# Optimization experiments

Measured on AMD Instinct MI355X. Metric: run time of the kernel, lower is better.

Reference implementation:

```python
import jax, jax.numpy as jnp
import numpy as np

PAD = 26
H = 1900
B = 256
T_EPI = 25
T_ANT = 64
T_TOT = 153
EMB = 10
IC = 2 * H  # classifier in_channels = 3800


def setup_inputs() -> dict:
    key = jax.random.key(0)
    ks = jax.random.split(key, 16)
    def rn(i, s, sc):
        return jax.random.normal(ks[i], s, jnp.float32) * sc
    inp = {
        "epitope_x": jax.random.randint(ks[0], (B, T_EPI), 0, 26),
        "left_antigen_x": jax.random.randint(ks[1], (B, T_ANT), 0, 26),
        "right_antigen_x": jax.random.randint(ks[2], (B, T_ANT), 0, 26),
        "total_antigen_x": jax.random.randint(ks[3], (B, T_TOT), 0, 26),
        "embed": rn(4, (27, EMB), 0.1),
        "wx": rn(5, (EMB, 4 * H), 0.1),
        "wh": rn(6, (H, 4 * H), 0.02),
        "wmx": rn(7, (EMB, H), 0.1),
        "wmh": rn(8, (H, H), 0.02),
        "b": rn(9, (4 * H,), 0.1),
        "gx": jnp.ones((4 * H,), jnp.float32),
        "gh": jnp.ones((4 * H,), jnp.float32),
        "gmx": jnp.ones((H,), jnp.float32),
        "gmh": jnp.ones((H,), jnp.float32),
        "bn1_gamma": jnp.ones((IC,), jnp.float32),
        "bn1_beta": jnp.zeros((IC,), jnp.float32),
        "bn1_mean": jnp.zeros((IC,), jnp.float32),
        "bn1_var": jnp.ones((IC,), jnp.float32),
        "W1": rn(10, (IC, IC // 10), 0.02),
        "b1": jnp.zeros((IC // 10,), jnp.float32),
        "bn2_gamma": jnp.ones((IC // 10,), jnp.float32),
        "bn2_beta": jnp.zeros((IC // 10,), jnp.float32),
        "bn2_mean": jnp.zeros((IC // 10,), jnp.float32),
        "bn2_var": jnp.ones((IC // 10,), jnp.float32),
        "W2": rn(11, (IC // 10, 1), 0.05),
        "b2": jnp.zeros((1,), jnp.float32),
    }
    return inp


def _wn(w, g):
    # tf.nn.l2_normalize(w, dim=0) * g  (eps 1e-12)
    return w * (g * jax.lax.rsqrt(jnp.maximum(jnp.sum(w * w, axis=0, keepdims=True), 1e-12)))


def _mlstm(xs, wx, wh, wmx, wmh, b):
    # xs: [T, B, E] -> hidden states [B, T, H]
    nB = xs.shape[1]
    def step(carry, x):
        c, h = carry
        m = (x @ wmx) * (h @ wmh)
        z = x @ wx + m @ wh + b
        i, f, o, u = jnp.split(z, 4, axis=1)
        c = jax.nn.sigmoid(f) * c + jax.nn.sigmoid(i) * jnp.tanh(u)
        h = jax.nn.sigmoid(o) * jnp.tanh(c)
        return (c, h), h
    init = (jnp.zeros((nB, H), xs.dtype), jnp.zeros((nB, H), xs.dtype))
    _, hs = jax.lax.scan(step, init, xs)
    return jnp.swapaxes(hs, 0, 1)


def _forward(epitope_x, left_antigen_x, right_antigen_x, total_antigen_x, embed,
             wx, wh, wmx, wmh, b, gx, gh, gmx, gmh,
             bn1_gamma, bn1_beta, bn1_mean, bn1_var, W1, b1,
             bn2_gamma, bn2_beta, bn2_mean, bn2_var, W2, b2):
    wxn = _wn(wx, gx); whn = _wn(wh, gh); wmxn = _wn(wmx, gmx); wmhn = _wn(wmh, gmh)
    epi_len = jnp.sum((epitope_x != PAD).astype(jnp.int32), axis=1)
    left_len = jnp.maximum(jnp.sum((left_antigen_x != PAD).astype(jnp.int32), axis=1), 1)
    right_len = jnp.maximum(jnp.sum((right_antigen_x != PAD).astype(jnp.int32), axis=1), 1)
    tot_len = epi_len + left_len + right_len
    epi_emb = embed[epitope_x]          # [B, 25, 10]
    tot_emb = embed[total_antigen_x]    # [B, 153, 10]
    epi_hs = _mlstm(jnp.swapaxes(epi_emb, 0, 1), wxn, whn, wmxn, wmhn, b)   # [B, 25, H]
    tot_hs = _mlstm(jnp.swapaxes(tot_emb, 0, 1), wxn, whn, wmxn, wmhn, b)   # [B, 153, H]
    ei = jnp.clip(epi_len - 1, 0, epi_hs.shape[1] - 1)
    ti = jnp.clip(tot_len - 1, 0, tot_hs.shape[1] - 1)
    epi_h = jnp.take_along_axis(epi_hs, ei[:, None, None], axis=1)[:, 0]
    tot_h = jnp.take_along_axis(tot_hs, ti[:, None, None], axis=1)[:, 0]
    x = jnp.concatenate([tot_h, epi_h], axis=-1)  # [B, 3800]
    lrelu = lambda v: jnp.where(v >= 0, v, 0.3 * v)
    bn = lambda v, g, bt, m, vv: (v - m) * jax.lax.rsqrt(vv + 1e-3) * g + bt
    x = bn(lrelu(x), bn1_gamma, bn1_beta, bn1_mean, bn1_var)
    x = x @ W1 + b1
    x = bn(lrelu(x), bn2_gamma, bn2_beta, bn2_mean, bn2_var)
    x = x @ W2 + b2
    return x.reshape(-1)


def reference(epitope_x, left_antigen_x, right_antigen_x, total_antigen_x, embed,
              wx, wh, wmx, wmh, b, gx, gh, gmx, gmh,
              bn1_gamma, bn1_beta, bn1_mean, bn1_var, W1, b1,
              bn2_gamma, bn2_beta, bn2_mean, bn2_var, W2, b2):
    return _forward(epitope_x, left_antigen_x, right_antigen_x, total_antigen_x, embed,
                    wx, wh, wmx, wmh, b, gx, gh, gmx, gmh,
                    bn1_gamma, bn1_beta, bn1_mean, bn1_var, W1, b1,
                    bn2_gamma, bn2_beta, bn2_mean, bn2_var, W2, b2)
```

## Files before the change

kernel.cpp:

```cpp
#include <hip/hip_runtime.h>


typedef _Float16 f16;
typedef _Float16 half8 __attribute__((ext_vector_type(8)));
typedef float f32x4 __attribute__((ext_vector_type(4)));

#define H_    1900
#define HP    1920
#define NKA   60
#define NKB   61
#define NKF   120
#define NR    512
#define TT    153
#define TE    25
#define EMB_  10
#define FCN   384

__device__ __forceinline__ float sigm(float x) {
  float p = __expf(-fabsf(x));
  float r = 1.f / (1.f + p);
  return x >= 0.f ? r : 1.f - r;
}
__device__ __forceinline__ float tanh_(float x) {
  float p = __expf(-2.f * fabsf(x));
  float r = (1.f - p) / (1.f + p);
  return x >= 0.f ? r : -r;
}

__device__ __forceinline__ void gll16(const f16* g, f16* l) {
  __builtin_amdgcn_global_load_lds(
      (const __attribute__((address_space(1))) unsigned int*)g,
      (__attribute__((address_space(3))) unsigned int*)l, 16, 0, 0);
}


__global__ void k_norms(const float* __restrict__ wh, const float* __restrict__ wx,
                        const float* __restrict__ wmh, const float* __restrict__ wmx,
                        const float* __restrict__ gh, const float* __restrict__ gx,
                        const float* __restrict__ gmh, const float* __restrict__ gmx,
                        float* __restrict__ inv_wh, float* __restrict__ inv_wx,
                        float* __restrict__ inv_wmh, float* __restrict__ inv_wmx) {
  int tid = blockIdx.x * 256 + threadIdx.x;
  if (tid < 7600) {
    float s = 0.f;
    for (int k = 0; k < H_; k++) { float v = wh[(size_t)k * 7600 + tid]; s += v * v; }
    inv_wh[tid] = gh[tid] * rsqrtf(fmaxf(s, 1e-12f));
  } else if (tid < 15200) {
    int n = tid - 7600; float s = 0.f;
    for (int e = 0; e < EMB_; e++) { float v = wx[(size_t)e * 7600 + n]; s += v * v; }
    inv_wx[n] = gx[n] * rsqrtf(fmaxf(s, 1e-12f));
  } else if (tid < 17100) {
    int n = tid - 15200; float s = 0.f;
    for (int k = 0; k < H_; k++) { float v = wmh[(size_t)k * H_ + n]; s += v * v; }
    inv_wmh[n] = gmh[n] * rsqrtf(fmaxf(s, 1e-12f));
  } else if (tid < 19000) {
    int n = tid - 17100; float s = 0.f;
    for (int e = 0; e < EMB_; e++) { float v = wmx[(size_t)e * H_ + n]; s += v * v; }
    inv_wmx[n] = gmx[n] * rsqrtf(fmaxf(s, 1e-12f));
  }
}

__global__ void k_wmhS(const float* __restrict__ wmh, const float* __restrict__ inv,
                       f16* __restrict__ WmhS) {
  int i = blockIdx.x * 256 + threadIdx.x;
  if (i >= 1920 * 1920) return;
  int n = i % 1920, k = i / 1920;
  float v = (n < H_ && k < H_) ? wmh[(size_t)k * H_ + n] * inv[n] : 0.f;
  int c = n >> 4, nl = n & 15, kb = k >> 5, kl = k & 31;
  WmhS[(((size_t)c * NKA + kb) * 512) + (nl + 16 * (kl >> 3)) * 8 + (kl & 7)] = (f16)v;
}

__global__ void k_whS(const float* __restrict__ wh, const float* __restrict__ wx,
                      const float* __restrict__ bias,
                      const float* __restrict__ inv_wh, const float* __restrict__ inv_wx,
                      f16* __restrict__ WhS) {
  int i = blockIdx.x * 256 + threadIdx.x;
  if (i >= 7600 * 1952) return;
  int col = i % 7600, k = i / 7600;
  float v = 0.f;
  if (k < H_)                        v = wh[(size_t)k * 7600 + col] * inv_wh[col];
  else if (k >= HP && k < HP + EMB_) v = wx[(size_t)(k - HP) * 7600 + col] * inv_wx[col];
  else if (k == HP + EMB_)           v = bias[col];
  int g = col / H_, n = col % H_;
  int q = n >> 4, nl = n & 15, kb = k >> 5, kl = k & 31;
  WhS[(((size_t)(q * 4 + g) * NKB + kb) * 512) + (nl + 16 * (kl >> 3)) * 8 + (kl & 7)] = (f16)v;
}

__global__ void k_wmxT(const float* __restrict__ wmx, const float* __restrict__ inv_wmx,
                       f16* __restrict__ wmxT) {
  int i = blockIdx.x * 256 + threadIdx.x;
  if (i >= HP * 32) return;
  int n = i >> 5, k = i & 31;
  float v = (k < EMB_ && n < H_) ? wmx[(size_t)k * H_ + n] * inv_wmx[n] : 0.f;
  wmxT[i] = (f16)v;
}

__global__ void k_lens(const int* __restrict__ ex, const int* __restrict__ lx,
                       const int* __restrict__ rx, int* __restrict__ sel) {
  int s = threadIdx.x;
  int el = 0; for (int i = 0; i < 25; i++) el += (ex[s * 25 + i] != 26);
  int ll = 0; for (int i = 0; i < 64; i++) ll += (lx[s * 64 + i] != 26);
  int rl = 0; for (int i = 0; i < 64; i++) rl += (rx[s * 64 + i] != 26);
  ll = ll < 1 ? 1 : ll;  rl = rl < 1 ? 1 : rl;
  int tl = el + ll + rl;
  int ti = tl - 1; ti = ti < 0 ? 0 : (ti > 152 ? 152 : ti);
  int ei = el - 1; ei = ei < 0 ? 0 : (ei > 24 ? 24 : ei);
  sel[s] = ti; sel[256 + s] = ei;
}

__global__ void k_init(f16* __restrict__ h0, f16* __restrict__ h1, float* __restrict__ c) {
  int i = blockIdx.x * 256 + threadIdx.x;
  if (i < NR * HP) { h0[i] = (f16)0.f; h1[i] = (f16)0.f; c[i] = 0.f; }
}

__global__ void k_xe16(const int* __restrict__ totx, const int* __restrict__ epix,
                       const float* __restrict__ embed, f16* __restrict__ xe16) {
  int i = blockIdx.x * blockDim.x + threadIdx.x;
  if (i >= TT * NR) return;
  int t = i / NR, r = i % NR;
  int tok = -1;
  if (r < 256) tok = totx[r * TT + t];
  else if (t < TE) tok = epix[(r - 256) * TE + t];
  f16* o = xe16 + (size_t)i * 32;
  #pragma unroll
  for (int e = 0; e < EMB_; e++) o[e] = (f16)(tok >= 0 ? embed[tok * EMB_ + e] : 0.f);
  o[10] = (f16)1.f;
  #pragma unroll
  for (int e = 11; e < 32; e++) o[e] = (f16)0.f;
}


__global__ __launch_bounds__(256, 1)
void k_stepA(const f16* __restrict__ hS, const f16* __restrict__ WmhS,
             const f16* __restrict__ xe16_t, const f16* __restrict__ wmxT,
             f16* __restrict__ mS, int rgc) {
  __shared__ __align__(16) f16 Bb[2][8][4][512];
  const int lane = threadIdx.x & 63, wid = threadIdx.x >> 6;
  const int bi = blockIdx.x;
  const int x = bi & 7, mm = bi >> 3;
  const int rg = mm % rgc, chi = mm / rgc;
  const int ct = chi * 8 + x;
  if (ct >= 30) return;
  const int rtile = rg * 4 + wid;
  const int r0 = rtile * 16;
  const int l16 = lane & 15, l4 = lane >> 4;

  const f16* Abase = hS   + (size_t)rtile * NKA * 512 + lane * 8;
  const f16* Bglob = WmhS + (size_t)(ct * 4) * NKA * 512 + lane * 8;

  f32x4 xm[4];
  {
    half8 xa = *(const half8*)(xe16_t + (size_t)(r0 + l16) * 32 + l4 * 8);
    #pragma unroll
    for (int cb = 0; cb < 4; cb++) {
      half8 xb = *(const half8*)(wmxT + (size_t)(ct * 64 + cb * 16 + l16) * 32 + l4 * 8);
      f32x4 z = {0.f, 0.f, 0.f, 0.f};
      xm[cb] = __builtin_amdgcn_mfma_f32_16x16x32_f16(xa, xb, z, 0, 0, 0);
    }
  }

  half8 Areg[2][8];
  f32x4 acc[4];
  #pragma unroll
  for (int cb = 0; cb < 4; cb++) { f32x4 z = {0.f, 0.f, 0.f, 0.f}; acc[cb] = z; }

#define STAGE_A(g, buf) { const int c0_ = (g) * 8, n_ = ((g) == 7 ? 4 : 8); \
    _Pragma("unroll") for (int q_ = 0; q_ < 8; q_++) { int p_ = wid * 8 + q_; \
      if (p_ < n_ * 4) { int kbl_ = p_ >> 2, cb_ = p_ & 3; \
        gll16(Bglob + ((size_t)cb_ * NKA + c0_ + kbl_) * 512, &Bb[buf][kbl_][cb_][0]); } } }
#define LOADA_A(g, buf) { const int c0_ = (g) * 8, n_ = ((g) == 7 ? 4 : 8); \
    _Pragma("unroll") for (int kk_ = 0; kk_ < 8; kk_++) if (kk_ < n_) \
      Areg[buf][kk_] = *(const half8*)(Abase + (size_t)(c0_ + kk_) * 512); }
#define COMP_A(g, buf) { const int n_ = ((g) == 7 ? 4 : 8); \
    _Pragma("unroll") for (int kk_ = 0; kk_ < 8; kk_++) if (kk_ < n_) { \
      half8 fbv0 = *(const half8*)&Bb[buf][kk_][0][lane * 8]; \
      half8 fbv1 = *(const half8*)&Bb[buf][kk_][1][lane * 8]; \
      half8 fbv2 = *(const half8*)&Bb[buf][kk_][2][lane * 8]; \
      half8 fbv3 = *(const half8*)&Bb[buf][kk_][3][lane * 8]; \
      acc[0] = __builtin_amdgcn_mfma_f32_16x16x32_f16(Areg[buf][kk_], fbv0, acc[0], 0, 0, 0); \
      acc[1] = __builtin_amdgcn_mfma_f32_16x16x32_f16(Areg[buf][kk_], fbv1, acc[1], 0, 0, 0); \
      acc[2] = __builtin_amdgcn_mfma_f32_16x16x32_f16(Areg[buf][kk_], fbv2, acc[2], 0, 0, 0); \
      acc[3] = __builtin_amdgcn_mfma_f32_16x16x32_f16(Areg[buf][kk_], fbv3, acc[3], 0, 0, 0); } }

  LOADA_A(0, 0); STAGE_A(0, 0);
  __syncthreads();
  #pragma unroll
  for (int g = 0; g < 8; g++) {
    if (g < 7) { STAGE_A(g + 1, (g + 1) & 1); LOADA_A(g + 1, (g + 1) & 1); }
    COMP_A(g, g & 1);
    __syncthreads();
  }
#undef STAGE_A
#undef LOADA_A
#undef COMP_A

  const int q4 = lane >> 4, c16 = lane & 15;
  #pragma unroll
  for (int cb = 0; cb < 4; cb++) {
    int kb = ct * 2 + (cb >> 1);
    int klane = (cb & 1) * 16 + c16;
    int lf = (klane >> 3) * 16;
    int sub = c16 & 7;
    f16* dst = mS + ((size_t)rtile * NKB + kb) * 512 + sub;
    #pragma unroll
    for (int q = 0; q < 4; q++) {
      int rl = q4 * 4 + q;
      dst[(rl + lf) * 8] = (f16)(acc[cb][q] * xm[cb][q]);
    }
  }
  if (ct == 0) {
    f16* dst = mS + ((size_t)rtile * NKB + 60) * 512 + lane * 8;
    *(half8*)dst = *(const half8*)(xe16_t + (size_t)(r0 + l16) * 32 + l4 * 8);
  }
}

__global__ __launch_bounds__(256, 1)
void k_stepB(const f16* __restrict__ mS, const f16* __restrict__ WhS,
             float* __restrict__ c, f16* __restrict__ houtS,
             float* __restrict__ selH, const int* __restrict__ sel, int t, int rgc) {
  __shared__ __align__(16) f16 Bb[2][8][4][512];
  const int lane = threadIdx.x & 63, wid = threadIdx.x >> 6;
  const int bi = blockIdx.x;
  const int x = bi & 7, mm = bi >> 3;
  const int rg = mm % rgc, chi = mm / rgc;
  const int colq = chi * 8 + x;
  if (colq >= 119) return;
  const int rt0 = (rg * 4 + wid) * 2;
  const int r0 = rt0 * 16;

  const f16* Abase = mS  + (size_t)rt0 * NKB * 512 + lane * 8;
  const f16* Bglob = WhS + (size_t)(colq * 4) * NKB * 512 + lane * 8;

  half8 Areg[2][8][2];
  f32x4 acc[2][4];
  #pragma unroll
  for (int a = 0; a < 2; a++)
    #pragma unroll
    for (int b = 0; b < 4; b++) { f32x4 z = {0.f, 0.f, 0.f, 0.f}; acc[a][b] = z; }

#define STAGE_B(g, buf) { const int c0_ = (g) * 8, n_ = ((g) == 7 ? 5 : 8); \
    _Pragma("unroll") for (int q_ = 0; q_ < 8; q_++) { int p_ = wid * 8 + q_; \
      if (p_ < n_ * 4) { int kbl_ = p_ >> 2, gg_ = p_ & 3; \
        gll16(Bglob + ((size_t)gg_ * NKB + c0_ + kbl_) * 512, &Bb[buf][kbl_][gg_][0]); } } }
#define LOADA_B(g, buf) { const int c0_ = (g) * 8, n_ = ((g) == 7 ? 5 : 8); \
    _Pragma("unroll") for (int kk_ = 0; kk_ < 8; kk_++) if (kk_ < n_) { \
      Areg[buf][kk_][0] = *(const half8*)(Abase + (size_t)(c0_ + kk_) * 512); \
      Areg[buf][kk_][1] = *(const half8*)(Abase + ((size_t)NKB + c0_ + kk_) * 512); } }
#define COMP_B(g, buf) { const int n_ = ((g) == 7 ? 5 : 8); \
    _Pragma("unroll") for (int kk_ = 0; kk_ < 8; kk_++) if (kk_ < n_) { \
      half8 fbv0 = *(const half8*)&Bb[buf][kk_][0][lane * 8]; \
      half8 fbv1 = *(const half8*)&Bb[buf][kk_][1][lane * 8]; \
      half8 fbv2 = *(const half8*)&Bb[buf][kk_][2][lane * 8]; \
      half8 fbv3 = *(const half8*)&Bb[buf][kk_][3][lane * 8]; \
      _Pragma("unroll") for (int rf_ = 0; rf_ < 2; rf_++) { \
        acc[rf_][0] = __builtin_amdgcn_mfma_f32_16x16x32_f16(Areg[buf][kk_][rf_], fbv0, acc[rf_][0], 0, 0, 0); \
        acc[rf_][1] = __builtin_amdgcn_mfma_f32_16x16x32_f16(Areg[buf][kk_][rf_], fbv1, acc[rf_][1], 0, 0, 0); \
        acc[rf_][2] = __builtin_amdgcn_mfma_f32_16x16x32_f16(Areg[buf][kk_][rf_], fbv2, acc[rf_][2], 0, 0, 0); \
        acc[rf_][3] = __builtin_amdgcn_mfma_f32_16x16x32_f16(Areg[buf][kk_][rf_], fbv3, acc[rf_][3], 0, 0, 0); } } }

  LOADA_B(0, 0); STAGE_B(0, 0);
  __syncthreads();
  #pragma unroll
  for (int g = 0; g < 8; g++) {
    if (g < 7) { STAGE_B(g + 1, (g + 1) & 1); LOADA_B(g + 1, (g + 1) & 1); }
    COMP_B(g, g & 1);
    __syncthreads();
  }
#undef STAGE_B
#undef LOADA_B
#undef COMP_B

  const int q4 = lane >> 4, c16 = lane & 15;
  const int j = colq * 16 + c16;
  const bool valid = j < H_;
  const int kbh = colq >> 1;
  const int lfh = ((((colq & 1) * 16 + c16) >> 3)) * 16;
  const int subh = c16 & 7;
  #pragma unroll
  for (int rf = 0; rf < 2; rf++) {
    f16* hdst = houtS + ((size_t)(rt0 + rf) * NKA + kbh) * 512 + subh;
    #pragma unroll
    for (int q = 0; q < 4; q++) {
      int rl = q4 * 4 + q;
      int row = r0 + rf * 16 + rl;
      if (valid) {
        size_t idx = (size_t)row * HP + j;
        float cold = c[idx];
        float iz = acc[rf][0][q], fz = acc[rf][1][q];
        float oz = acc[rf][2][q], uz = acc[rf][3][q];
        float cn = sigm(fz) * cold + sigm(iz) * tanh_(uz);
        float hv = sigm(oz) * tanh_(cn);
        c[idx] = cn;
        hdst[(rl + lfh) * 8] = (f16)hv;
        if (t == sel[row]) selH[idx] = hv;
      }
    }
  }
}


__global__ void k_xqS(const float* __restrict__ selH, const float* __restrict__ g1,
                      const float* __restrict__ be1, const float* __restrict__ mu1,
                      const float* __restrict__ var1, f16* __restrict__ xqS) {
  int i = blockIdx.x * 256 + threadIdx.x;
  if (i >= 256 * 3840) return;
  int k = i % 3840, s = i / 3840;
  float v = 0.f; bool have = false;
  if (k < H_)            { v = selH[(size_t)s * HP + k]; have = true; }
  else if (k < 2 * H_)   { v = selH[(size_t)(256 + s) * HP + (k - H_)]; have = true; }
  float q = 0.f;
  if (have) {
    float lr = v < 0.f ? 0.3f * v : v;
    q = (lr - mu1[k]) * rsqrtf(var1[k] + 1e-3f) * g1[k] + be1[k];
  }
  int rtile = s >> 4, sl = s & 15, kb = k >> 5, kl = k & 31;
  xqS[(((size_t)rtile * NKF + kb) * 512) + (sl + 16 * (kl >> 3)) * 8 + (kl & 7)] = (f16)q;
}

__global__ void k_w1S(const float* __restrict__ W1, f16* __restrict__ W1S) {
  int i = blockIdx.x * 256 + threadIdx.x;
  if (i >= 384 * 3840) return;
  int col = i % 384, k = i / 384;
  float v = (col < 380 && k < 2 * H_) ? W1[(size_t)k * 380 + col] : 0.f;
  int cg = col >> 4, nl = col & 15, kb = k >> 5, kl = k & 31;
  W1S[(((size_t)cg * NKF + kb) * 512) + (nl + 16 * (kl >> 3)) * 8 + (kl & 7)] = (f16)v;
}

__global__ __launch_bounds__(256)
void k_fc1(const f16* __restrict__ xqS, const f16* __restrict__ W1S,
           const float* __restrict__ b1, float* __restrict__ z1) {
  const int lane = threadIdx.x & 63, wid = threadIdx.x >> 6;
  const int ct = blockIdx.x % 6, rg = blockIdx.x / 6;
  const int rtile = rg * 4 + wid;
  const int r0 = rtile * 16;

  const f16* Abase = xqS + (size_t)rtile * NKF * 512 + lane * 8;
  const f16* Bbase = W1S + (size_t)(ct * 4) * NKF * 512 + lane * 8;

  half8 fa0, fa1, fa2, fa3;
  half8 fb0[4], fb1[4], fb2[4], fb3[4];
  f32x4 acc[4];
  #pragma unroll
  for (int cb = 0; cb < 4; cb++) { f32x4 z = {0.f, 0.f, 0.f, 0.f}; acc[cb] = z; }

#define LDA_F(d, kb)  d = *(const half8*)(Abase + (size_t)(kb) * 512)
#define LDB_F(d, kb)  { _Pragma("unroll") for (int cb = 0; cb < 4; cb++) \
    d[cb] = *(const half8*)(Bbase + ((size_t)cb * NKF + (kb)) * 512); }
#define MMA_F(fa, fb) { _Pragma("unroll") for (int cb = 0; cb < 4; cb++) \
    acc[cb] = __builtin_amdgcn_mfma_f32_16x16x32_f16(fa, fb[cb], acc[cb], 0, 0, 0); }

// ... 37 lines not shown
                      const float* __restrict__ b2, float* __restrict__ out) {
  int s = threadIdx.x;
  float a = 0.f;
  for (int jj = 0; jj < 380; jj++) {
    float v = z1[(size_t)s * FCN + jj];
    float lr = v < 0.f ? 0.3f * v : v;
    float q = (lr - mu2[jj]) * rsqrtf(var2[jj] + 1e-3f) * g2[jj] + be2[jj];
    a += q * W2[jj];
  }
  out[s] = a + b2[0];
}


extern "C" void kernel_launch(void* const* d_in, const int* in_sizes, int n_in,
                              void* d_out, int out_size, void* d_ws, size_t ws_size,
                              hipStream_t stream) {
  const int*   epix  = (const int*)d_in[0];
  const int*   lx    = (const int*)d_in[1];
  const int*   rx    = (const int*)d_in[2];
  const int*   totx  = (const int*)d_in[3];
  const float* embed = (const float*)d_in[4];
  const float* wx    = (const float*)d_in[5];
  const float* wh    = (const float*)d_in[6];
  const float* wmx   = (const float*)d_in[7];
  const float* wmh   = (const float*)d_in[8];
  const float* bb    = (const float*)d_in[9];
  const float* gx    = (const float*)d_in[10];
  const float* gh    = (const float*)d_in[11];
  const float* gmx   = (const float*)d_in[12];
  const float* gmh   = (const float*)d_in[13];
  const float* bn1g  = (const float*)d_in[14];
  const float* bn1b  = (const float*)d_in[15];
  const float* bn1m  = (const float*)d_in[16];
  const float* bn1v  = (const float*)d_in[17];
  const float* W1    = (const float*)d_in[18];
  const float* b1    = (const float*)d_in[19];
  const float* bn2g  = (const float*)d_in[20];
  const float* bn2b  = (const float*)d_in[21];
  const float* bn2m  = (const float*)d_in[22];
  const float* bn2v  = (const float*)d_in[23];
  const float* W2    = (const float*)d_in[24];
  const float* b2v   = (const float*)d_in[25];

  char* base = (char*)d_ws;
  size_t off = 0;
  auto alloc = [&](size_t n) { char* p = base + off; off = (off + n + 255) & ~(size_t)255; return p; };

  f16*   WmhS   = (f16*)  alloc((size_t)120 * NKA * 512 * 2);
  f16*   WhS    = (f16*)  alloc((size_t)119 * 4 * NKB * 512 * 2);
  f16*   wmxT   = (f16*)  alloc((size_t)HP * 32 * 2);
  f16*   xe16   = (f16*)  alloc((size_t)TT * NR * 32 * 2);
  f16*   h0S    = (f16*)  alloc((size_t)32 * NKA * 512 * 2);
  f16*   h1S    = (f16*)  alloc((size_t)32 * NKA * 512 * 2);
  f16*   mS     = (f16*)  alloc((size_t)32 * NKB * 512 * 2);
  float* cst    = (float*)alloc((size_t)NR * HP * 4);
  float* selH   = (float*)alloc((size_t)NR * HP * 4);
  int*   sel    = (int*)  alloc((size_t)NR * 4);
  float* inv_wh = (float*)alloc(7600 * 4);
  float* inv_wx = (float*)alloc(7600 * 4);
  float* inv_wmh= (float*)alloc(1900 * 4);
  float* inv_wmx= (float*)alloc(1900 * 4);
  f16*   xqS    = (f16*)  alloc((size_t)16 * NKF * 512 * 2);
  f16*   W1S    = (f16*)  alloc((size_t)24 * NKF * 512 * 2);
  float* z1     = (float*)alloc((size_t)256 * FCN * 4);
  (void)in_sizes; (void)n_in; (void)out_size; (void)ws_size;

  hipLaunchKernelGGL(k_norms, dim3(75), dim3(256), 0, stream,
                     wh, wx, wmh, wmx, gh, gx, gmh, gmx, inv_wh, inv_wx, inv_wmh, inv_wmx);
  hipLaunchKernelGGL(k_wmhS, dim3((1920 * 1920 + 255) / 256), dim3(256), 0, stream,
                     wmh, inv_wmh, WmhS);
  hipLaunchKernelGGL(k_whS, dim3((7600 * 1952 + 255) / 256), dim3(256), 0, stream,
                     wh, wx, bb, inv_wh, inv_wx, WhS);
  hipLaunchKernelGGL(k_wmxT, dim3((HP * 32 + 255) / 256), dim3(256), 0, stream,
                     wmx, inv_wmx, wmxT);
  hipLaunchKernelGGL(k_lens, dim3(1), dim3(256), 0, stream, epix, lx, rx, sel);
  hipLaunchKernelGGL(k_init, dim3((NR * HP + 255) / 256), dim3(256), 0, stream,
                     h0S, h1S, cst);
  hipLaunchKernelGGL(k_xe16, dim3((TT * NR + 255) / 256), dim3(256), 0, stream,
                     totx, epix, embed, xe16);

  for (int t = 0; t < TT; t++) {
    int Mt = (t < TE) ? NR : 256;
    const f16* hin = (t & 1) ? h1S : h0S;
    f16*       ho  = (t & 1) ? h0S : h1S;
    int rgcA = Mt / 64;
    int rgcB = Mt / 128;
    hipLaunchKernelGGL(k_stepA, dim3(8 * rgcA * 4), dim3(256), 0, stream,
                       hin, WmhS, xe16 + (size_t)t * NR * 32, wmxT, mS, rgcA);
    hipLaunchKernelGGL(k_stepB, dim3(8 * rgcB * 15), dim3(256), 0, stream,
                       mS, WhS, cst, ho, selH, sel, t, rgcB);
  }

  hipLaunchKernelGGL(k_xqS, dim3((256 * 3840 + 255) / 256), dim3(256), 0, stream,
                     selH, bn1g, bn1b, bn1m, bn1v, xqS);
  hipLaunchKernelGGL(k_w1S, dim3((384 * 3840 + 255) / 256), dim3(256), 0, stream, W1, W1S);
  hipLaunchKernelGGL(k_fc1, dim3(24), dim3(256), 0, stream, xqS, W1S, b1, z1);
  hipLaunchKernelGGL(k_fc2, dim3(1), dim3(256), 0, stream,
                     z1, bn2g, bn2b, bn2m, bn2v, W2, b2v, (float*)d_out);
}
```

Baseline: 5.279 ms.

## Triple-buffer LDS weight tiles with explicit vmcnt waits in step kernels

Both recurrent GEMM step kernels move from a double-buffered loop to a fully unrolled three-stage LDS pipeline. Weight tiles are prefetched two groups ahead with global_load_lds, and A fragments alternate between two register sets. Each __syncthreads is replaced by a partial s_waitcnt vmcnt plus s_barrier, so later loads can stay in flight while the current group computes. The cost is 50% more LDS and hand-counted vmcnt values that must exactly match the number of issued loads.

```diff
diff --git a/kernel.cpp b/kernel.cpp
--- a/kernel.cpp
+++ b/kernel.cpp
@@ -15,6 +15,11 @@
 #define TE    25
 #define EMB_  10
 #define FCN   384
+
+#define WAITV(n) do { asm volatile("s_waitcnt vmcnt(" #n ")" ::: "memory"); \
+                      __builtin_amdgcn_sched_barrier(0); } while (0)
+#define BARR  do { __builtin_amdgcn_s_barrier(); \
+                   __builtin_amdgcn_sched_barrier(0); } while (0)
 
 __device__ __forceinline__ float sigm(float x) {
   float p = __expf(-fabsf(x));
@@ -134,7 +139,7 @@
 void k_stepA(const f16* __restrict__ hS, const f16* __restrict__ WmhS,
              const f16* __restrict__ xe16_t, const f16* __restrict__ wmxT,
              f16* __restrict__ mS, int rgc) {
-  __shared__ __align__(16) f16 Bb[2][8][4][512];
+  __shared__ __align__(16) f16 Bb[3][8][4][512];
   const int lane = threadIdx.x & 63, wid = threadIdx.x >> 6;
   const int bi = blockIdx.x;
   const int x = bi & 7, mm = bi >> 3;
@@ -158,41 +163,40 @@
       xm[cb] = __builtin_amdgcn_mfma_f32_16x16x32_f16(xa, xb, z, 0, 0, 0);
     }
   }
-
-  half8 Areg[2][8];
+  WAITV(0);
+
+  half8 Areg0[8], Areg1[8];
   f32x4 acc[4];
   #pragma unroll
   for (int cb = 0; cb < 4; cb++) { f32x4 z = {0.f, 0.f, 0.f, 0.f}; acc[cb] = z; }
 
-#define STAGE_A(g, buf) { const int c0_ = (g) * 8, n_ = ((g) == 7 ? 4 : 8); \
-    _Pragma("unroll") for (int q_ = 0; q_ < 8; q_++) { int p_ = wid * 8 + q_; \
-      if (p_ < n_ * 4) { int kbl_ = p_ >> 2, cb_ = p_ & 3; \
-        gll16(Bglob + ((size_t)cb_ * NKA + c0_ + kbl_) * 512, &Bb[buf][kbl_][cb_][0]); } } }
-#define LOADA_A(g, buf) { const int c0_ = (g) * 8, n_ = ((g) == 7 ? 4 : 8); \
-    _Pragma("unroll") for (int kk_ = 0; kk_ < 8; kk_++) if (kk_ < n_) \
-      Areg[buf][kk_] = *(const half8*)(Abase + (size_t)(c0_ + kk_) * 512); }
-#define COMP_A(g, buf) { const int n_ = ((g) == 7 ? 4 : 8); \
-    _Pragma("unroll") for (int kk_ = 0; kk_ < 8; kk_++) if (kk_ < n_) { \
-      half8 fbv0 = *(const half8*)&Bb[buf][kk_][0][lane * 8]; \
-      half8 fbv1 = *(const half8*)&Bb[buf][kk_][1][lane * 8]; \
-      half8 fbv2 = *(const half8*)&Bb[buf][kk_][2][lane * 8]; \
-      half8 fbv3 = *(const half8*)&Bb[buf][kk_][3][lane * 8]; \
-      acc[0] = __builtin_amdgcn_mfma_f32_16x16x32_f16(Areg[buf][kk_], fbv0, acc[0], 0, 0, 0); \
-      acc[1] = __builtin_amdgcn_mfma_f32_16x16x32_f16(Areg[buf][kk_], fbv1, acc[1], 0, 0, 0); \
-      acc[2] = __builtin_amdgcn_mfma_f32_16x16x32_f16(Areg[buf][kk_], fbv2, acc[2], 0, 0, 0); \
-      acc[3] = __builtin_amdgcn_mfma_f32_16x16x32_f16(Areg[buf][kk_], fbv3, acc[3], 0, 0, 0); } }
-
-  LOADA_A(0, 0); STAGE_A(0, 0);
-  __syncthreads();
-  #pragma unroll
-  for (int g = 0; g < 8; g++) {
-    if (g < 7) { STAGE_A(g + 1, (g + 1) & 1); LOADA_A(g + 1, (g + 1) & 1); }
-    COMP_A(g, g & 1);
-    __syncthreads();
-  }
-#undef STAGE_A
-#undef LOADA_A
-#undef COMP_A
+#define S_A(g, buf, n) { _Pragma("unroll") for (int q_ = 0; q_ < (n); q_++) { \
+    int p_ = wid * (n) + q_; int kbl_ = p_ >> 2, cb_ = p_ & 3; \
+    gll16(Bglob + ((size_t)cb_ * NKA + (g) * 8 + kbl_) * 512, &Bb[buf][kbl_][cb_][0]); } }
+#define A_A(g, ab, n) { _Pragma("unroll") for (int kk_ = 0; kk_ < 8; kk_++) if (kk_ < (n)) \
+    Areg##ab[kk_] = *(const half8*)(Abase + (size_t)((g) * 8 + kk_) * 512); }
+#define C_A(g, buf, ab, n) { _Pragma("unroll") for (int kk_ = 0; kk_ < 8; kk_++) if (kk_ < (n)) { \
+    half8 b0_ = *(const half8*)&Bb[buf][kk_][0][lane * 8]; \
+    half8 b1_ = *(const half8*)&Bb[buf][kk_][1][lane * 8]; \
+    half8 b2_ = *(const half8*)&Bb[buf][kk_][2][lane * 8]; \
+    half8 b3_ = *(const half8*)&Bb[buf][kk_][3][lane * 8]; \
+    acc[0] = __builtin_amdgcn_mfma_f32_16x16x32_f16(Areg##ab[kk_], b0_, acc[0], 0, 0, 0); \
+    acc[1] = __builtin_amdgcn_mfma_f32_16x16x32_f16(Areg##ab[kk_], b1_, acc[1], 0, 0, 0); \
+    acc[2] = __builtin_amdgcn_mfma_f32_16x16x32_f16(Areg##ab[kk_], b2_, acc[2], 0, 0, 0); \
+    acc[3] = __builtin_amdgcn_mfma_f32_16x16x32_f16(Areg##ab[kk_], b3_, acc[3], 0, 0, 0); } }
+
+  S_A(0, 0, 8); S_A(1, 1, 8); A_A(0, 0, 8);
+  A_A(1, 1, 8); S_A(2, 2, 8); WAITV(16); BARR; C_A(0, 0, 0, 8); BARR;
+  A_A(2, 0, 8); S_A(3, 0, 8); WAITV(24); BARR; C_A(1, 1, 1, 8); BARR;
+  A_A(3, 1, 8); S_A(4, 1, 8); WAITV(24); BARR; C_A(2, 2, 0, 8); BARR;
+  A_A(4, 0, 8); S_A(5, 2, 8); WAITV(24); BARR; C_A(3, 0, 1, 8); BARR;
+  A_A(5, 1, 8); S_A(6, 0, 8); WAITV(24); BARR; C_A(4, 1, 0, 8); BARR;
+  A_A(6, 0, 8); S_A(7, 1, 4); WAITV(20); BARR; C_A(5, 2, 1, 8); BARR;
+  A_A(7, 1, 4); WAITV(8);  BARR; C_A(6, 0, 0, 8); BARR;
+  WAITV(0); BARR; C_A(7, 1, 1, 4);
+#undef S_A
+#undef A_A
+#undef C_A
 
   const int q4 = lane >> 4, c16 = lane & 15;
   #pragma unroll
@@ -218,7 +222,7 @@
 void k_stepB(const f16* __restrict__ mS, const f16* __restrict__ WhS,
              float* __restrict__ c, f16* __restrict__ houtS,
              float* __restrict__ selH, const int* __restrict__ sel, int t, int rgc) {
-  __shared__ __align__(16) f16 Bb[2][8][4][512];
+  __shared__ __align__(16) f16 Bb[3][8][4][512];
   const int lane = threadIdx.x & 63, wid = threadIdx.x >> 6;
   const int bi = blockIdx.x;
   const int x = bi & 7, mm = bi >> 3;
@@ -231,44 +235,42 @@
   const f16* Abase = mS  + (size_t)rt0 * NKB * 512 + lane * 8;
   const f16* Bglob = WhS + (size_t)(colq * 4) * NKB * 512 + lane * 8;
 
-  half8 Areg[2][8][2];
+  half8 Areg0[8][2], Areg1[8][2];
   f32x4 acc[2][4];
   #pragma unroll
   for (int a = 0; a < 2; a++)
     #pragma unroll
     for (int b = 0; b < 4; b++) { f32x4 z = {0.f, 0.f, 0.f, 0.f}; acc[a][b] = z; }
 
-#define STAGE_B(g, buf) { const int c0_ = (g) * 8, n_ = ((g) == 7 ? 5 : 8); \
-    _Pragma("unroll") for (int q_ = 0; q_ < 8; q_++) { int p_ = wid * 8 + q_; \
-      if (p_ < n_ * 4) { int kbl_ = p_ >> 2, gg_ = p_ & 3; \
-        gll16(Bglob + ((size_t)gg_ * NKB + c0_ + kbl_) * 512, &Bb[buf][kbl_][gg_][0]); } } }
-#define LOADA_B(g, buf) { const int c0_ = (g) * 8, n_ = ((g) == 7 ? 5 : 8); \
-    _Pragma("unroll") for (int kk_ = 0; kk_ < 8; kk_++) if (kk_ < n_) { \
-      Areg[buf][kk_][0] = *(const half8*)(Abase + (size_t)(c0_ + kk_) * 512); \
-      Areg[buf][kk_][1] = *(const half8*)(Abase + ((size_t)NKB + c0_ + kk_) * 512); } }
-#define COMP_B(g, buf) { const int n_ = ((g) == 7 ? 5 : 8); \
-    _Pragma("unroll") for (int kk_ = 0; kk_ < 8; kk_++) if (kk_ < n_) { \
-      half8 fbv0 = *(const half8*)&Bb[buf][kk_][0][lane * 8]; \
-      half8 fbv1 = *(const half8*)&Bb[buf][kk_][1][lane * 8]; \
-      half8 fbv2 = *(const half8*)&Bb[buf][kk_][2][lane * 8]; \
-      half8 fbv3 = *(const half8*)&Bb[buf][kk_][3][lane * 8]; \
-      _Pragma("unroll") for (int rf_ = 0; rf_ < 2; rf_++) { \
-        acc[rf_][0] = __builtin_amdgcn_mfma_f32_16x16x32_f16(Areg[buf][kk_][rf_], fbv0, acc[rf_][0], 0, 0, 0); \
-        acc[rf_][1] = __builtin_amdgcn_mfma_f32_16x16x32_f16(Areg[buf][kk_][rf_], fbv1, acc[rf_][1], 0, 0, 0); \
-        acc[rf_][2] = __builtin_amdgcn_mfma_f32_16x16x32_f16(Areg[buf][kk_][rf_], fbv2, acc[rf_][2], 0, 0, 0); \
-        acc[rf_][3] = __builtin_amdgcn_mfma_f32_16x16x32_f16(Areg[buf][kk_][rf_], fbv3, acc[rf_][3], 0, 0, 0); } } }
-
-  LOADA_B(0, 0); STAGE_B(0, 0);
-  __syncthreads();
-  #pragma unroll
-  for (int g = 0; g < 8; g++) {
-    if (g < 7) { STAGE_B(g + 1, (g + 1) & 1); LOADA_B(g + 1, (g + 1) & 1); }
-    COMP_B(g, g & 1);
-    __syncthreads();
-  }
-#undef STAGE_B
-#undef LOADA_B
-#undef COMP_B
+#define S_B(g, buf, n) { _Pragma("unroll") for (int q_ = 0; q_ < (n); q_++) { \
+    int p_ = wid * (n) + q_; int kbl_ = p_ >> 2, gg_ = p_ & 3; \
+    gll16(Bglob + ((size_t)gg_ * NKB + (g) * 8 + kbl_) * 512, &Bb[buf][kbl_][gg_][0]); } }
+#define A_B(g, ab, n) { _Pragma("unroll") for (int kk_ = 0; kk_ < 8; kk_++) if (kk_ < (n)) { \
+    Areg##ab[kk_][0] = *(const half8*)(Abase + (size_t)((g) * 8 + kk_) * 512); \
+    Areg##ab[kk_][1] = *(const half8*)(Abase + ((size_t)NKB + (g) * 8 + kk_) * 512); } }
+#define C_B(g, buf, ab, n) { _Pragma("unroll") for (int kk_ = 0; kk_ < 8; kk_++) if (kk_ < (n)) { \
+    half8 b0_ = *(const half8*)&Bb[buf][kk_][0][lane * 8]; \
+    half8 b1_ = *(const half8*)&Bb[buf][kk_][1][lane * 8]; \
+    half8 b2_ = *(const half8*)&Bb[buf][kk_][2][lane * 8]; \
+    half8 b3_ = *(const half8*)&Bb[buf][kk_][3][lane * 8]; \
+    _Pragma("unroll") for (int rf_ = 0; rf_ < 2; rf_++) { \
+      acc[rf_][0] = __builtin_amdgcn_mfma_f32_16x16x32_f16(Areg##ab[kk_][rf_], b0_, acc[rf_][0], 0, 0, 0); \
+      acc[rf_][1] = __builtin_amdgcn_mfma_f32_16x16x32_f16(Areg##ab[kk_][rf_], b1_, acc[rf_][1], 0, 0, 0); \
+      acc[rf_][2] = __builtin_amdgcn_mfma_f32_16x16x32_f16(Areg##ab[kk_][rf_], b2_, acc[rf_][2], 0, 0, 0); \
+      acc[rf_][3] = __builtin_amdgcn_mfma_f32_16x16x32_f16(Areg##ab[kk_][rf_], b3_, acc[rf_][3], 0, 0, 0); } } }
+
+  S_B(0, 0, 8); S_B(1, 1, 8); A_B(0, 0, 8);
+  A_B(1, 1, 8); S_B(2, 2, 8); WAITV(24); BARR; C_B(0, 0, 0, 8); BARR;
+  A_B(2, 0, 8); S_B(3, 0, 8); WAITV(32); BARR; C_B(1, 1, 1, 8); BARR;
+  A_B(3, 1, 8); S_B(4, 1, 8); WAITV(32); BARR; C_B(2, 2, 0, 8); BARR;
+  A_B(4, 0, 8); S_B(5, 2, 8); WAITV(32); BARR; C_B(3, 0, 1, 8); BARR;
+  A_B(5, 1, 8); S_B(6, 0, 8); WAITV(32); BARR; C_B(4, 1, 0, 8); BARR;
+  A_B(6, 0, 8); S_B(7, 1, 5); WAITV(29); BARR; C_B(5, 2, 1, 8); BARR;
+  A_B(7, 1, 5); WAITV(15); BARR; C_B(6, 0, 0, 8); BARR;
+  WAITV(0); BARR; C_B(7, 1, 1, 5);
+#undef S_B
+#undef A_B
+#undef C_B
 
   const int q4 = lane >> 4, c16 = lane & 15;
   const int j = colq * 16 + c16;
```

Measured after the change: 5.371 ms. About the same (+1.7%).

## Fuse LSTM step kernels into persistent kernel with grid barriers, two steps per launch

Applied to the files above, without the earlier changes.

Replaces the per-timestep pair of launches (m-projection GEMM, then gate GEMM plus cell update) with one persistent 256-block kernel. Each launch handles two timesteps and separates phases with an atomic-counter grid barrier. Work items are strided over the fixed grid, and a second m buffer avoids overwriting between the fused steps. The aim is to cut kernel-launch and drain overhead across the 153 sequential steps. In exchange it relies on all 256 blocks being co-resident, and the spin barrier adds its own latency.

```diff
diff --git a/kernel.cpp b/kernel.cpp
--- a/kernel.cpp
+++ b/kernel.cpp
@@ -15,6 +15,7 @@
 #define TE    25
 #define EMB_  10
 #define FCN   384
+#define NBLK  256
 
 __device__ __forceinline__ float sigm(float x) {
   float p = __expf(-fabsf(x));
@@ -31,6 +32,19 @@
   __builtin_amdgcn_global_load_lds(
       (const __attribute__((address_space(1))) unsigned int*)g,
       (__attribute__((address_space(3))) unsigned int*)l, 16, 0, 0);
+}
+
+__device__ __forceinline__ void gsync(int* flag) {
+  asm volatile("s_waitcnt vmcnt(0)" ::: "memory");
+  __syncthreads();
+  if (threadIdx.x == 0) {
+    __hip_atomic_fetch_add(flag, 1, __ATOMIC_RELEASE, __HIP_MEMORY_SCOPE_AGENT);
+    while (__hip_atomic_load(flag, __ATOMIC_RELAXED, __HIP_MEMORY_SCOPE_AGENT) < NBLK) {
+      __builtin_amdgcn_s_sleep(2);
+    }
+  }
+  __syncthreads();
+  asm volatile("" ::: "memory");
 }
 
 
@@ -108,9 +122,11 @@
   sel[s] = ti; sel[256 + s] = ei;
 }
 
-__global__ void k_init(f16* __restrict__ h0, f16* __restrict__ h1, float* __restrict__ c) {
+__global__ void k_init(f16* __restrict__ h0, f16* __restrict__ h1,
+                       float* __restrict__ c, int* __restrict__ flags) {
   int i = blockIdx.x * 256 + threadIdx.x;
   if (i < NR * HP) { h0[i] = (f16)0.f; h1[i] = (f16)0.f; c[i] = 0.f; }
+  if (i < 256) flags[i] = 0;
 }
 
 __global__ void k_xe16(const int* __restrict__ totx, const int* __restrict__ epix,
@@ -131,171 +147,194 @@
 
 
 __global__ __launch_bounds__(256, 1)
-void k_stepA(const f16* __restrict__ hS, const f16* __restrict__ WmhS,
-             const f16* __restrict__ xe16_t, const f16* __restrict__ wmxT,
-             f16* __restrict__ mS, int rgc) {
+void k_step2(const f16* __restrict__ WmhS, const f16* __restrict__ WhS,
+             const f16* __restrict__ wmxT, const f16* __restrict__ xe16,
+             f16* __restrict__ h0S, f16* __restrict__ h1S,
+             f16* __restrict__ mS0, f16* __restrict__ mS1,
+             float* __restrict__ cst, float* __restrict__ selH,
+             const int* __restrict__ sel, int* __restrict__ flag3,
+             int t0, int ns) {
   __shared__ __align__(16) f16 Bb[2][8][4][512];
   const int lane = threadIdx.x & 63, wid = threadIdx.x >> 6;
-  const int bi = blockIdx.x;
-  const int x = bi & 7, mm = bi >> 3;
-  const int rg = mm % rgc, chi = mm / rgc;
-  const int ct = chi * 8 + x;
-  if (ct >= 30) return;
-  const int rtile = rg * 4 + wid;
-  const int r0 = rtile * 16;
+  const int x = blockIdx.x & 7, m = blockIdx.x >> 3;
   const int l16 = lane & 15, l4 = lane >> 4;
-
-  const f16* Abase = hS   + (size_t)rtile * NKA * 512 + lane * 8;
-  const f16* Bglob = WmhS + (size_t)(ct * 4) * NKA * 512 + lane * 8;
-
-  f32x4 xm[4];
-  {
-    half8 xa = *(const half8*)(xe16_t + (size_t)(r0 + l16) * 32 + l4 * 8);
-    #pragma unroll
-    for (int cb = 0; cb < 4; cb++) {
-      half8 xb = *(const half8*)(wmxT + (size_t)(ct * 64 + cb * 16 + l16) * 32 + l4 * 8);
-      f32x4 z = {0.f, 0.f, 0.f, 0.f};
-      xm[cb] = __builtin_amdgcn_mfma_f32_16x16x32_f16(xa, xb, z, 0, 0, 0);
+  const int q4 = l4, c16 = l16;
+  int bar = 0;
+
+#define STAGE_A(g, buf, n_) { _Pragma("unroll") for (int q_ = 0; q_ < 8; q_++) { \
+    int p_ = wid * 8 + q_; \
+    if (p_ < (n_) * 4) { int kbl_ = p_ >> 2, cb_ = p_ & 3; \
+      gll16(BglobA + ((size_t)cb_ * NKA + (g) * 8 + kbl_) * 512, &Bb[buf][kbl_][cb_][0]); } } }
+#define LOADA_A(g, buf, n_) { _Pragma("unroll") for (int kk_ = 0; kk_ < 8; kk_++) if (kk_ < (n_)) \
+    ArA[buf][kk_] = *(const half8*)(AbaseA + (size_t)((g) * 8 + kk_) * 512); }
+#define COMP_A(g, buf, n_) { _Pragma("unroll") for (int kk_ = 0; kk_ < 8; kk_++) if (kk_ < (n_)) { \
+    half8 b0_ = *(const half8*)&Bb[buf][kk_][0][lane * 8]; \
+    half8 b1_ = *(const half8*)&Bb[buf][kk_][1][lane * 8]; \
+    half8 b2_ = *(const half8*)&Bb[buf][kk_][2][lane * 8]; \
+    half8 b3_ = *(const half8*)&Bb[buf][kk_][3][lane * 8]; \
+    accA[0] = __builtin_amdgcn_mfma_f32_16x16x32_f16(ArA[buf][kk_], b0_, accA[0], 0, 0, 0); \
+    accA[1] = __builtin_amdgcn_mfma_f32_16x16x32_f16(ArA[buf][kk_], b1_, accA[1], 0, 0, 0); \
+    accA[2] = __builtin_amdgcn_mfma_f32_16x16x32_f16(ArA[buf][kk_], b2_, accA[2], 0, 0, 0); \
+    accA[3] = __builtin_amdgcn_mfma_f32_16x16x32_f16(ArA[buf][kk_], b3_, accA[3], 0, 0, 0); } }
+
+#define STAGE_B(g, buf, n_) { _Pragma("unroll") for (int q_ = 0; q_ < 8; q_++) { \
+    int p_ = wid * 8 + q_; \
+    if (p_ < (n_) * 4) { int kbl_ = p_ >> 2, gg_ = p_ & 3; \
+      gll16(BglobB + ((size_t)gg_ * NKB + (g) * 8 + kbl_) * 512, &Bb[buf][kbl_][gg_][0]); } } }
+#define LOADA_B(g, buf, n_) { _Pragma("unroll") for (int kk_ = 0; kk_ < 8; kk_++) if (kk_ < (n_)) { \
+    ArB[buf][kk_][0] = *(const half8*)(AbaseB + (size_t)((g) * 8 + kk_) * 512); \
+    ArB[buf][kk_][1] = *(const half8*)(AbaseB + ((size_t)NKB + (g) * 8 + kk_) * 512); } }
+#define COMP_B(g, buf, n_) { _Pragma("unroll") for (int kk_ = 0; kk_ < 8; kk_++) if (kk_ < (n_)) { \
+    half8 b0_ = *(const half8*)&Bb[buf][kk_][0][lane * 8]; \
+    half8 b1_ = *(const half8*)&Bb[buf][kk_][1][lane * 8]; \
+    half8 b2_ = *(const half8*)&Bb[buf][kk_][2][lane * 8]; \
+    half8 b3_ = *(const half8*)&Bb[buf][kk_][3][lane * 8]; \
+    _Pragma("unroll") for (int rf_ = 0; rf_ < 2; rf_++) { \
+      accB[rf_][0] = __builtin_amdgcn_mfma_f32_16x16x32_f16(ArB[buf][kk_][rf_], b0_, accB[rf_][0], 0, 0, 0); \
+      accB[rf_][1] = __builtin_amdgcn_mfma_f32_16x16x32_f16(ArB[buf][kk_][rf_], b1_, accB[rf_][1], 0, 0, 0); \
+      accB[rf_][2] = __builtin_amdgcn_mfma_f32_16x16x32_f16(ArB[buf][kk_][rf_], b2_, accB[rf_][2], 0, 0, 0); \
+      accB[rf_][3] = __builtin_amdgcn_mfma_f32_16x16x32_f16(ArB[buf][kk_][rf_], b3_, accB[rf_][3], 0, 0, 0); } } }
+
+  for (int s = 0; s < ns; s++) {
+    const int t = t0 + s;
+    const int Mt = (t < TE) ? NR : 256;
+    const f16* hS = (t & 1) ? h1S : h0S;
+    f16* ho = (t & 1) ? h0S : h1S;
+    f16* mS = s ? mS1 : mS0;
+    const f16* xet = xe16 + (size_t)t * NR * 32;
+    const int rgcA = Mt / 64, rgcB = Mt / 128;
+
+    {
+      const int nct = (x < 6) ? 4 : 3;
+      const int itemsA = nct * rgcA;
+      for (int it = m; it < itemsA; it += 32) {
+        const int ct = (it / rgcA) * 8 + x;
+        const int rg = it % rgcA;
+        const int rtile = rg * 4 + wid;
+        const int r0 = rtile * 16;
+
+        const f16* AbaseA = hS   + (size_t)rtile * NKA * 512 + lane * 8;
+        const f16* BglobA = WmhS + (size_t)(ct * 4) * NKA * 512 + lane * 8;
+
+        f32x4 xm[4];
+        {
+          half8 xa = *(const half8*)(xet + (size_t)(r0 + l16) * 32 + l4 * 8);
+          #pragma unroll
+          for (int cb = 0; cb < 4; cb++) {
+            half8 xb = *(const half8*)(wmxT + (size_t)(ct * 64 + cb * 16 + l16) * 32 + l4 * 8);
+            f32x4 z = {0.f, 0.f, 0.f, 0.f};
+            xm[cb] = __builtin_amdgcn_mfma_f32_16x16x32_f16(xa, xb, z, 0, 0, 0);
+          }
+        }
+
+        half8 ArA[2][8];
+        f32x4 accA[4];
+        #pragma unroll
+        for (int cb = 0; cb < 4; cb++) { f32x4 z = {0.f, 0.f, 0.f, 0.f}; accA[cb] = z; }
+
+        LOADA_A(0, 0, 8); STAGE_A(0, 0, 8);
+        __syncthreads();
+        #pragma unroll
+        for (int g = 0; g < 8; g++) {
+          const int nn = (g == 7) ? 4 : 8;
+          if (g < 7) {
+            const int nn1 = (g == 6) ? 4 : 8;
+            STAGE_A(g + 1, (g + 1) & 1, nn1); LOADA_A(g + 1, (g + 1) & 1, nn1);
+          }
+          COMP_A(g, g & 1, nn);
+          __syncthreads();
+        }
+
+        #pragma unroll
+        for (int cb = 0; cb < 4; cb++) {
+          int kb = ct * 2 + (cb >> 1);
+          int klane = (cb & 1) * 16 + c16;
+          int lf = (klane >> 3) * 16;
+          int sub = c16 & 7;
+          f16* dst = mS + ((size_t)rtile * NKB + kb) * 512 + sub;
+          #pragma unroll
+          for (int q = 0; q < 4; q++) {
+            int rl = q4 * 4 + q;
+            dst[(rl + lf) * 8] = (f16)(accA[cb][q] * xm[cb][q]);
+          }
+        }
+        if (ct == 0) {
+          f16* dst = mS + ((size_t)rtile * NKB + 60) * 512 + lane * 8;
+          *(half8*)dst = *(const half8*)(xet + (size_t)(r0 + l16) * 32 + l4 * 8);
+        }
+      }
     }
-  }
-
-  half8 Areg[2][8];
-  f32x4 acc[4];
-  #pragma unroll
-  for (int cb = 0; cb < 4; cb++) { f32x4 z = {0.f, 0.f, 0.f, 0.f}; acc[cb] = z; }
-
-#define STAGE_A(g, buf) { const int c0_ = (g) * 8, n_ = ((g) == 7 ? 4 : 8); \
-    _Pragma("unroll") for (int q_ = 0; q_ < 8; q_++) { int p_ = wid * 8 + q_; \
-      if (p_ < n_ * 4) { int kbl_ = p_ >> 2, cb_ = p_ & 3; \
-        gll16(Bglob + ((size_t)cb_ * NKA + c0_ + kbl_) * 512, &Bb[buf][kbl_][cb_][0]); } } }
-#define LOADA_A(g, buf) { const int c0_ = (g) * 8, n_ = ((g) == 7 ? 4 : 8); \
-    _Pragma("unroll") for (int kk_ = 0; kk_ < 8; kk_++) if (kk_ < n_) \
-      Areg[buf][kk_] = *(const half8*)(Abase + (size_t)(c0_ + kk_) * 512); }
-#define COMP_A(g, buf) { const int n_ = ((g) == 7 ? 4 : 8); \
-    _Pragma("unroll") for (int kk_ = 0; kk_ < 8; kk_++) if (kk_ < n_) { \
-      half8 fbv0 = *(const half8*)&Bb[buf][kk_][0][lane * 8]; \
-      half8 fbv1 = *(const half8*)&Bb[buf][kk_][1][lane * 8]; \
-      half8 fbv2 = *(const half8*)&Bb[buf][kk_][2][lane * 8]; \
-      half8 fbv3 = *(const half8*)&Bb[buf][kk_][3][lane * 8]; \
-      acc[0] = __builtin_amdgcn_mfma_f32_16x16x32_f16(Areg[buf][kk_], fbv0, acc[0], 0, 0, 0); \
-      acc[1] = __builtin_amdgcn_mfma_f32_16x16x32_f16(Areg[buf][kk_], fbv1, acc[1], 0, 0, 0); \
-      acc[2] = __builtin_amdgcn_mfma_f32_16x16x32_f16(Areg[buf][kk_], fbv2, acc[2], 0, 0, 0); \
-      acc[3] = __builtin_amdgcn_mfma_f32_16x16x32_f16(Areg[buf][kk_], fbv3, acc[3], 0, 0, 0); } }
-
-  LOADA_A(0, 0); STAGE_A(0, 0);
-  __syncthreads();
-  #pragma unroll
-  for (int g = 0; g < 8; g++) {
-    if (g < 7) { STAGE_A(g + 1, (g + 1) & 1); LOADA_A(g + 1, (g + 1) & 1); }
-    COMP_A(g, g & 1);
-    __syncthreads();
+
+    gsync(flag3 + bar); bar++;
+
+    {
+      const int ncq = (x == 7) ? 14 : 15;
+      const int itemsB = ncq * rgcB;
+      for (int it = m; it < itemsB; it += 32) {
+        const int colq = (it / rgcB) * 8 + x;
+        const int rg = it % rgcB;
+        const int rt0 = (rg * 4 + wid) * 2;
+        const int r0 = rt0 * 16;
+
+        const f16* AbaseB = mS  + (size_t)rt0 * NKB * 512 + lane * 8;
+        const f16* BglobB = WhS + (size_t)(colq * 4) * NKB * 512 + lane * 8;
+
+        half8 ArB[2][8][2];
+        f32x4 accB[2][4];
+        #pragma unroll
+        for (int a = 0; a < 2; a++)
+          #pragma unroll
+          for (int b = 0; b < 4; b++) { f32x4 z = {0.f, 0.f, 0.f, 0.f}; accB[a][b] = z; }
+
+        LOADA_B(0, 0, 8); STAGE_B(0, 0, 8);
+        __syncthreads();
+        #pragma unroll
+        for (int g = 0; g < 8; g++) {
+          const int nn = (g == 7) ? 5 : 8;
+          if (g < 7) {
+            const int nn1 = (g == 6) ? 5 : 8;
+            STAGE_B(g + 1, (g + 1) & 1, nn1); LOADA_B(g + 1, (g + 1) & 1, nn1);
+          }
+          COMP_B(g, g & 1, nn);
+          __syncthreads();
+        }
+
+        const int j = colq * 16 + c16;
+        const bool valid = j < H_;
+        const int kbh = colq >> 1;
+        const int lfh = ((((colq & 1) * 16 + c16) >> 3)) * 16;
+        const int subh = c16 & 7;
+        #pragma unroll
+        for (int rf = 0; rf < 2; rf++) {
+          f16* hdst = ho + ((size_t)(rt0 + rf) * NKA + kbh) * 512 + subh;
+          #pragma unroll
+          for (int q = 0; q < 4; q++) {
+            int rl = q4 * 4 + q;
+            int row = r0 + rf * 16 + rl;
+            if (valid) {
+              size_t idx = (size_t)row * HP + j;
+              float cold = cst[idx];
+              float iz = accB[rf][0][q], fz = accB[rf][1][q];
+              float oz = accB[rf][2][q], uz = accB[rf][3][q];
+              float cn = sigm(fz) * cold + sigm(iz) * tanh_(uz);
+              float hv = sigm(oz) * tanh_(cn);
+              cst[idx] = cn;
+              hdst[(rl + lfh) * 8] = (f16)hv;
+              if (t == sel[row]) selH[idx] = hv;
+            }
+          }
+        }
+      }
+    }
+
+    if (s + 1 < ns) { gsync(flag3 + bar); bar++; }
   }
 #undef STAGE_A
 #undef LOADA_A
 #undef COMP_A
-
-  const int q4 = lane >> 4, c16 = lane & 15;
-  #pragma unroll
-  for (int cb = 0; cb < 4; cb++) {
-    int kb = ct * 2 + (cb >> 1);
-    int klane = (cb & 1) * 16 + c16;
-    int lf = (klane >> 3) * 16;
-    int sub = c16 & 7;
-    f16* dst = mS + ((size_t)rtile * NKB + kb) * 512 + sub;
-    #pragma unroll
-    for (int q = 0; q < 4; q++) {
-      int rl = q4 * 4 + q;
-      dst[(rl + lf) * 8] = (f16)(acc[cb][q] * xm[cb][q]);
-    }
-  }
-  if (ct == 0) {
-    f16* dst = mS + ((size_t)rtile * NKB + 60) * 512 + lane * 8;
-    *(half8*)dst = *(const half8*)(xe16_t + (size_t)(r0 + l16) * 32 + l4 * 8);
-  }
-}
-
-__global__ __launch_bounds__(256, 1)
-void k_stepB(const f16* __restrict__ mS, const f16* __restrict__ WhS,
-             float* __restrict__ c, f16* __restrict__ houtS,
-             float* __restrict__ selH, const int* __restrict__ sel, int t, int rgc) {
-  __shared__ __align__(16) f16 Bb[2][8][4][512];
-  const int lane = threadIdx.x & 63, wid = threadIdx.x >> 6;
-  const int bi = blockIdx.x;
-  const int x = bi & 7, mm = bi >> 3;
-  const int rg = mm % rgc, chi = mm / rgc;
-  const int colq = chi * 8 + x;
-  if (colq >= 119) return;
-  const int rt0 = (rg * 4 + wid) * 2;
-  const int r0 = rt0 * 16;
-
-  const f16* Abase = mS  + (size_t)rt0 * NKB * 512 + lane * 8;
-  const f16* Bglob = WhS + (size_t)(colq * 4) * NKB * 512 + lane * 8;
-
-  half8 Areg[2][8][2];
-  f32x4 acc[2][4];
-  #pragma unroll
-  for (int a = 0; a < 2; a++)
-    #pragma unroll
-    for (int b = 0; b < 4; b++) { f32x4 z = {0.f, 0.f, 0.f, 0.f}; acc[a][b] = z; }
-
-#define STAGE_B(g, buf) { const int c0_ = (g) * 8, n_ = ((g) == 7 ? 5 : 8); \
-    _Pragma("unroll") for (int q_ = 0; q_ < 8; q_++) { int p_ = wid * 8 + q_; \
-      if (p_ < n_ * 4) { int kbl_ = p_ >> 2, gg_ = p_ & 3; \
-        gll16(Bglob + ((size_t)gg_ * NKB + c0_ + kbl_) * 512, &Bb[buf][kbl_][gg_][0]); } } }
-#define LOADA_B(g, buf) { const int c0_ = (g) * 8, n_ = ((g) == 7 ? 5 : 8); \
-    _Pragma("unroll") for (int kk_ = 0; kk_ < 8; kk_++) if (kk_ < n_) { \
-      Areg[buf][kk_][0] = *(const half8*)(Abase + (size_t)(c0_ + kk_) * 512); \
-      Areg[buf][kk_][1] = *(const half8*)(Abase + ((size_t)NKB + c0_ + kk_) * 512); } }
-#define COMP_B(g, buf) { const int n_ = ((g) == 7 ? 5 : 8); \
-    _Pragma("unroll") for (int kk_ = 0; kk_ < 8; kk_++) if (kk_ < n_) { \
-      half8 fbv0 = *(const half8*)&Bb[buf][kk_][0][lane * 8]; \
-      half8 fbv1 = *(const half8*)&Bb[buf][kk_][1][lane * 8]; \
-      half8 fbv2 = *(const half8*)&Bb[buf][kk_][2][lane * 8]; \
-      half8 fbv3 = *(const half8*)&Bb[buf][kk_][3][lane * 8]; \
-      _Pragma("unroll") for (int rf_ = 0; rf_ < 2; rf_++) { \
-        acc[rf_][0] = __builtin_amdgcn_mfma_f32_16x16x32_f16(Areg[buf][kk_][rf_], fbv0, acc[rf_][0], 0, 0, 0); \
-        acc[rf_][1] = __builtin_amdgcn_mfma_f32_16x16x32_f16(Areg[buf][kk_][rf_], fbv1, acc[rf_][1], 0, 0, 0); \
-        acc[rf_][2] = __builtin_amdgcn_mfma_f32_16x16x32_f16(Areg[buf][kk_][rf_], fbv2, acc[rf_][2], 0, 0, 0); \
-        acc[rf_][3] = __builtin_amdgcn_mfma_f32_16x16x32_f16(Areg[buf][kk_][rf_], fbv3, acc[rf_][3], 0, 0, 0); } } }
-
-  LOADA_B(0, 0); STAGE_B(0, 0);
-  __syncthreads();
-  #pragma unroll
-  for (int g = 0; g < 8; g++) {
-    if (g < 7) { STAGE_B(g + 1, (g + 1) & 1); LOADA_B(g + 1, (g + 1) & 1); }
-    COMP_B(g, g & 1);
-    __syncthreads();
-  }
 #undef STAGE_B
 #undef LOADA_B
 #undef COMP_B
-
-  const int q4 = lane >> 4, c16 = lane & 15;
-  const int j = colq * 16 + c16;
-  const bool valid = j < H_;
-  const int kbh = colq >> 1;
-  const int lfh = ((((colq & 1) * 16 + c16) >> 3)) * 16;
-  const int subh = c16 & 7;
-  #pragma unroll
-  for (int rf = 0; rf < 2; rf++) {
-    f16* hdst = houtS + ((size_t)(rt0 + rf) * NKA + kbh) * 512 + subh;
-    #pragma unroll
-    for (int q = 0; q < 4; q++) {
-      int rl = q4 * 4 + q;
-      int row = r0 + rf * 16 + rl;
-      if (valid) {
-        size_t idx = (size_t)row * HP + j;
-        float cold = c[idx];
-        float iz = acc[rf][0][q], fz = acc[rf][1][q];
-        float oz = acc[rf][2][q], uz = acc[rf][3][q];
-        float cn = sigm(fz) * cold + sigm(iz) * tanh_(uz);
-        float hv = sigm(oz) * tanh_(cn);
-        c[idx] = cn;
-        hdst[(rl + lfh) * 8] = (f16)hv;
-        if (t == sel[row]) selH[idx] = hv;
-      }
-    }
-  }
 }
 
 
@@ -439,7 +478,8 @@
   f16*   xe16   = (f16*)  alloc((size_t)TT * NR * 32 * 2);
   f16*   h0S    = (f16*)  alloc((size_t)32 * NKA * 512 * 2);
   f16*   h1S    = (f16*)  alloc((size_t)32 * NKA * 512 * 2);
-  f16*   mS     = (f16*)  alloc((size_t)32 * NKB * 512 * 2);
+  f16*   mS0    = (f16*)  alloc((size_t)32 * NKB * 512 * 2);
+  f16*   mS1    = (f16*)  alloc((size_t)32 * NKB * 512 * 2);
   float* cst    = (float*)alloc((size_t)NR * HP * 4);
   float* selH   = (float*)alloc((size_t)NR * HP * 4);
   int*   sel    = (int*)  alloc((size_t)NR * 4);
@@ -450,6 +490,7 @@
   f16*   xqS    = (f16*)  alloc((size_t)16 * NKF * 512 * 2);
   f16*   W1S    = (f16*)  alloc((size_t)24 * NKF * 512 * 2);
   float* z1     = (float*)alloc((size_t)256 * FCN * 4);
+  int*   flags  = (int*)  alloc(256 * 4);
   (void)in_sizes; (void)n_in; (void)out_size; (void)ws_size;
 
   hipLaunchKernelGGL(k_norms, dim3(75), dim3(256), 0, stream,
@@ -462,20 +503,15 @@
                      wmx, inv_wmx, wmxT);
   hipLaunchKernelGGL(k_lens, dim3(1), dim3(256), 0, stream, epix, lx, rx, sel);
   hipLaunchKernelGGL(k_init, dim3((NR * HP + 255) / 256), dim3(256), 0, stream,
-                     h0S, h1S, cst);
+                     h0S, h1S, cst, flags);
   hipLaunchKernelGGL(k_xe16, dim3((TT * NR + 255) / 256), dim3(256), 0, stream,
                      totx, epix, embed, xe16);
 
-  for (int t = 0; t < TT; t++) {
-    int Mt = (t < TE) ? NR : 256;
-    const f16* hin = (t & 1) ? h1S : h0S;
-    f16*       ho  = (t & 1) ? h0S : h1S;
-    int rgcA = Mt / 64;
-    int rgcB = Mt / 128;
-    hipLaunchKernelGGL(k_stepA, dim3(8 * rgcA * 4), dim3(256), 0, stream,
-                       hin, WmhS, xe16 + (size_t)t * NR * 32, wmxT, mS, rgcA);
-    hipLaunchKernelGGL(k_stepB, dim3(8 * rgcB * 15), dim3(256), 0, stream,
-                       mS, WhS, cst, ho, selH, sel, t, rgcB);
+  for (int t0 = 0; t0 < TT; t0 += 2) {
+    int ns = (t0 + 1 < TT) ? 2 : 1;
+    hipLaunchKernelGGL(k_step2, dim3(NBLK), dim3(256), 0, stream,
+                       WmhS, WhS, wmxT, xe16, h0S, h1S, mS0, mS1,
+                       cst, selH, sel, flags + (t0 / 2) * 3, t0, ns);
   }
 
   hipLaunchKernelGGL(k_xqS, dim3((256 * 3840 + 255) / 256), dim3(256), 0, stream,
```

Measured after the change: 7.549 ms. +43.0%, slower.
